# Kernel optimization log

Measured on AMD Instinct MI355X. Metric: run time of the kernel, lower is better.

Reference implementation:

```python
import jax, jax.numpy as jnp
import numpy as np
from jax import lax

E = 256          # embed_dim
D = 2 * E        # d_model
V = 100000       # num_symbols (pad idx = V)
B = 2048         # query batch
NB = 30          # fixed neighbor window (hardcoded in source)
FEW = 3          # hardcoded support set size (view(3,1,2E))
STEPS = 4        # query encoder process steps
EPS = 1e-3       # LayerNormalization eps


def setup_inputs() -> dict:
    key = jax.random.key(0)
    ks = iter(jax.random.split(key, 48))
    def n(shape, s=0.05):
        return jax.random.normal(next(ks), shape, jnp.float32) * s
    inp = {}
    inp["query"] = n((B, D))
    inp["support"] = n((FEW, D))
    inp["query_left_connections"] = jax.random.randint(next(ks), (B, NB, 2), 0, V)
    inp["query_left_degrees"] = jax.random.randint(next(ks), (B,), 1, NB)
    inp["query_right_connections"] = jax.random.randint(next(ks), (B, NB, 2), 0, V)
    inp["query_right_degrees"] = jax.random.randint(next(ks), (B,), 1, NB)
    inp["support_left_connections"] = jax.random.randint(next(ks), (FEW, NB, 2), 0, V)
    inp["support_left_degrees"] = jax.random.randint(next(ks), (FEW,), 1, NB)
    inp["support_right_connections"] = jax.random.randint(next(ks), (FEW, NB, 2), 0, V)
    inp["support_right_degrees"] = jax.random.randint(next(ks), (FEW,), 1, NB)
    # parameters
    inp["emb"] = n((V + 1, E), 0.02).at[V].set(0.0)   # padding_idx row = 0
    inp["naW"] = n((E, D)); inp["naB"] = jnp.zeros((E,), jnp.float32)
    inp["nuW"] = n((1, E)); inp["nuB"] = jnp.zeros((1,), jnp.float32)
    inp["p1W"] = n((2 * D, D)); inp["p1b"] = jnp.zeros((2 * D,), jnp.float32)
    inp["p2W"] = n((D, 2 * D)); inp["p2b"] = jnp.zeros((D,), jnp.float32)
    inp["lnA"] = jnp.ones((D,), jnp.float32); inp["lnB"] = jnp.zeros((D,), jnp.float32)
    inp["encWih"] = n((4 * D, D)); inp["encWhh"] = n((4 * D, D))
    inp["encBih"] = jnp.zeros((4 * D,), jnp.float32); inp["encBhh"] = jnp.zeros((4 * D,), jnp.float32)
    inp["decWih"] = n((4 * D, D)); inp["decWhh"] = n((4 * D, D))
    inp["decBih"] = jnp.zeros((4 * D,), jnp.float32); inp["decBhh"] = jnp.zeros((4 * D,), jnp.float32)
    inp["saW"] = n((E, D)); inp["saB"] = jnp.zeros((E,), jnp.float32)
    inp["suW"] = n((1, E)); inp["suB"] = jnp.zeros((1,), jnp.float32)
    inp["qWih"] = n((8 * D, D)); inp["qWhh"] = n((8 * D, 2 * D))
    inp["qBih"] = jnp.zeros((8 * D,), jnp.float32); inp["qBhh"] = jnp.zeros((8 * D,), jnp.float32)
    return inp


def _lstm_cell(x, h, c, Wih, Whh, bih, bhh):
    g = x @ Wih.T + bih + h @ Whh.T + bhh
    i, f, gg, o = jnp.split(g, 4, axis=-1)
    c = jax.nn.sigmoid(f) * c + jax.nn.sigmoid(i) * jnp.tanh(gg)
    h = jax.nn.sigmoid(o) * jnp.tanh(c)
    return h, c


def _layer_norm(z, a, b):
    # torch.std is unbiased (ddof=1); eps is added to sigma, not variance
    mu = jnp.mean(z, axis=-1, keepdims=True)
    sigma = jnp.std(z, axis=-1, keepdims=True, ddof=1)
    return (z - mu) / (sigma + EPS) * a + b


def _neighbor_encoder(conn, emb, naW, naB, nuW, nuB):
    rel = emb[conn[..., 0]]                 # [N,30,E] gather
    ent = emb[conn[..., 1]]                 # [N,30,E] gather
    cat = jnp.concatenate([rel, ent], -1)   # [N,30,2E]
    out = jnp.tanh(cat @ naW.T + naB)       # [N,30,E]
    att = jax.nn.softmax(out @ nuW.T + nuB, axis=1)  # softmax over 30 neighbors
    agg = jnp.einsum('nk,nke->ne', att[..., 0], ent)  # weighted bmm reduce
    return jnp.tanh(agg)


def _support_encoder(x, p1W, p1b, p2W, p2b, lnA, lnB):
    h = jax.nn.relu(x @ p1W.T + p1b)
    o = h @ p2W.T + p2b
    return _layer_norm(o + x, lnA, lnB)


def reference(query, support,
              query_left_connections, query_left_degrees,
              query_right_connections, query_right_degrees,
              support_left_connections, support_left_degrees,
              support_right_connections, support_right_degrees,
              emb, naW, naB, nuW, nuB, p1W, p1b, p2W, p2b, lnA, lnB,
              encWih, encWhh, encBih, encBhh, decWih, decWhh, decBih, decBhh,
              saW, saB, suW, suB, qWih, qWhh, qBih, qBhh):
    ne = lambda c: _neighbor_encoder(c, emb, naW, naB, nuW, nuB)
    query_neighbor = jnp.concatenate([ne(query_left_connections), ne(query_right_connections)], -1)    # [B,2E]
    support_neighbor = jnp.concatenate([ne(support_left_connections), ne(support_right_connections)], -1)  # [3,2E]

    support_g = _support_encoder(support_neighbor, p1W, p1b, p2W, p2b, lnA, lnB)  # [3,D]
    query_g = _support_encoder(query_neighbor, p1W, p1b, p2W, p2b, lnA, lnB)      # [B,D]

    # set autoencoder: LSTM over the 3 support vectors (seq=3, batch=1)
    support_g_0 = support_g.reshape(FEW, 1, D)
    def enc_step(carry, x):
        h, c = carry
        h, c = _lstm_cell(x, h, c, encWih, encWhh, encBih, encBhh)
        return (h, c), h
    z = jnp.zeros((1, D), support_g.dtype)
    (h_f, c_f), enc_out = lax.scan(enc_step, (z, z), support_g_0)  # enc_out [3,1,D]

    # decoder: feed back its own output 3 times, init from encoder state
    h_d, c_d = h_f, c_f
    x = enc_out[-1]
    outs = []
    for _ in range(FEW):
        h_d, c_d = _lstm_cell(x, h_d, c_d, decWih, decWhh, decBih, decBhh)
        outs.append(h_d)
        x = h_d
    decoder_set = jnp.stack(outs)  # [3,1,D]
    ae_loss = jnp.mean((support_g_0 - lax.stop_gradient(decoder_set)) ** 2)

    sge = support_g_0.reshape(FEW, D) + enc_out.reshape(FEW, D)
    satt = jnp.tanh(sge @ saW.T + saB)                       # [3,E]
    aw = jax.nn.softmax(satt @ suW.T + suB, axis=1)          # softmax over dim of size 1 -> ones (faithful)
    support_g_encoder = (sge.T @ aw).T.reshape(1, D)         # [1,D]

    # query encoder: LSTMCell(D -> 2D) process loop
    h_r = jnp.zeros((query_g.shape[0], 2 * D), query_g.dtype)
    c = jnp.zeros_like(h_r)
    for _ in range(STEPS):
        h_r_, c = _lstm_cell(query_g, h_r, c, qWih, qWhh, qBih, qBhh)
        h = query_g + h_r_[:, :D]
        attn = jax.nn.softmax(h @ support_g_encoder.T, axis=1)  # [B,1] -> ones (faithful)
        r = attn @ support_g_encoder                            # [B,D]
        h_r = jnp.concatenate([h, r], axis=1)
    query_f = h

    matching_scores = (query_f @ support_g_encoder.T)[:, 0]    # [B]
    return (matching_scores, ae_loss, support_g_encoder, query_g)
```

## Files before the change

kernel.cpp:

```cpp
#include <hip/hip_runtime.h>
#include <hip/hip_bf16.h>

typedef unsigned short u16;
typedef __attribute__((ext_vector_type(8))) short bf16x8;
typedef __attribute__((ext_vector_type(4))) float f32x4;
#define MFMA16(a,b,c) __builtin_amdgcn_mfma_f32_16x16x32_bf16(a,b,c,0,0,0)
#define VPAD 100000

__device__ __forceinline__ float sigf(float x){ return 1.0f/(1.0f + __expf(-x)); }
__device__ __forceinline__ float ftanh(float x){
    float ax = fabsf(x);
    float e = __expf(-2.f*ax);
    float r = (1.f - e) / (1.f + e);
    return copysignf(r, x);
}
__device__ __forceinline__ u16 f2b(float f){
    unsigned u = __float_as_uint(f);
    u += 0x7fffu + ((u >> 16) & 1u);
    return (u16)(u >> 16);
}
__device__ __forceinline__ unsigned int pk2(float x, float y){
    return ((unsigned)f2b(y) << 16) | (unsigned)f2b(x);
}
__device__ __forceinline__ float b2f(u16 u){
    return __uint_as_float(((unsigned int)u) << 16);
}
__device__ __forceinline__ uint4 pk8(float4 x, float4 y){
    uint4 o;
    o.x = pk2(x.x,x.y); o.y = pk2(x.z,x.w);
    o.z = pk2(y.x,y.y); o.w = pk2(y.z,y.w);
    return o;
}

__global__ __launch_bounds__(256) void prep_kernel(
    const float* __restrict__ p1W, const float* __restrict__ p2W,
    const float* __restrict__ naW,
    const float* __restrict__ qWih, const float* __restrict__ qWhh,
    const float* __restrict__ qBih, const float* __restrict__ qBhh,
    u16* __restrict__ p1Wb, u16* __restrict__ p2Wb,
    u16* __restrict__ nawf, u16* __restrict__ WihS, u16* __restrict__ WhhS,
    float* __restrict__ bc)
{
    const long gid = (long)blockIdx.x * 256 + threadIdx.x;
    const long E0 = 131072;
    const long E1 = E0 + 131072;
    const long E2 = E1 + 131072;
    const long E3 = E2 + 131072;
    const long E4 = E3 + 16384;
    const long E5 = E4 + 2048;
    if (gid < E0){
        float4 v = reinterpret_cast<const float4*>(p1W)[gid];
        uint2 s; s.x = pk2(v.x,v.y); s.y = pk2(v.z,v.w);
        reinterpret_cast<uint2*>(p1Wb)[gid] = s;
    } else if (gid < E1){
        long i = gid - E0;
        float4 v = reinterpret_cast<const float4*>(p2W)[i];
        uint2 s; s.x = pk2(v.x,v.y); s.y = pk2(v.z,v.w);
        reinterpret_cast<uint2*>(p2Wb)[i] = s;
    } else if (gid < E2){
        long j = gid - E1;
        int n = (int)(j >> 6), c8 = (int)(j & 63);
        int srow = (n & 3) * 1024 + (n >> 2);
        const float* sp = qWih + (size_t)srow * 512 + c8 * 8;
        float4 a = *reinterpret_cast<const float4*>(sp);
        float4 b = *reinterpret_cast<const float4*>(sp + 4);
        *reinterpret_cast<uint4*>(WihS + (size_t)n*512 + c8*8) = pk8(a,b);
    } else if (gid < E3){
        long j = gid - E2;
        int n = (int)(j >> 6), c8 = (int)(j & 63);
        int srow = (n & 3) * 1024 + (n >> 2);
        const float* sp = qWhh + (size_t)srow * 1024 + c8 * 8;
        float4 a = *reinterpret_cast<const float4*>(sp);
        float4 b = *reinterpret_cast<const float4*>(sp + 4);
        *reinterpret_cast<uint4*>(WhhS + (size_t)n*512 + c8*8) = pk8(a,b);
    } else if (gid < E4){
        long j = gid - E3;
        int f = (int)(j >> 6), lane = (int)(j & 63);
        int ks = f >> 4, ig = f & 15;
        int col = lane & 15, quad = lane >> 4;
        int n = ig*16 + col;
        int k0 = ks*32 + quad*8;
        const float* sp = naW + (size_t)n*512 + k0;
        float4 a = *reinterpret_cast<const float4*>(sp);
        float4 b = *reinterpret_cast<const float4*>(sp + 4);
        *reinterpret_cast<uint4*>(nawf + j*8) = pk8(a,b);
    } else if (gid < E5){
        int n = (int)(gid - E4);
        int row = (n & 3) * 1024 + (n >> 2);
        bc[n] = qBih[row] + qBhh[row];
    }
}

__global__ __launch_bounds__(256) void neighbor_v4(
    const int* __restrict__ qL, const int* __restrict__ qR,
    const int* __restrict__ sL, const int* __restrict__ sR,
    const float* __restrict__ emb,
    const u16* __restrict__ nawf,
    const float* __restrict__ naB, const float* __restrict__ nuW,
    const float* __restrict__ nuB,
    float* __restrict__ out, u16* __restrict__ out_bf)
{
    __shared__ __align__(16) u16 frg[32*512];
    __shared__ int relid[2][32];
    __shared__ int entid[2][32];
    __shared__ float logit[2][32];
    __shared__ float att[2][32];

    const int t = threadIdx.x;
    const int row = blockIdx.x;
    if (t < 128){
        int s = t >> 6, j = t & 63;
        int k = j >> 1, which = j & 1;
        const int* conn;
        if (row < 2048) conn = (s ? qR : qL) + (size_t)row * 60;
        else            conn = (s ? sR : sL) + (size_t)(row - 2048) * 60;
        int id = (k < 30) ? conn[k*2 + which] : VPAD;
        if (which) entid[s][k] = id; else relid[s][k] = id;
    }
    if (t >= 128 && t < 192){ int s = (t-128) >> 5; logit[s][(t-128)&31] = 0.f; }
    __syncthreads();

    const int w = t >> 6, lane = t & 63;
    const int col = lane & 15, quad = lane >> 4;

    int gc[8], gk[8], gs[8];
    #pragma unroll
    for (int i = 0; i < 8; i++){
        int idx = i*256 + t;
        gc[i] = idx & 31;
        gk[i] = (idx >> 5) & 31;
        gs[i] = idx >> 10;
    }

    f32x4 acc[4][4] = {};

    #pragma unroll
    for (int p = 0; p < 2; p++){
        #pragma unroll
        for (int i = 0; i < 8; i++){
            int s = gs[i], k = gk[i], c = gc[i];
            int e0 = c*8;
            int id = p ? entid[s][k] : relid[s][k];
            const float* ptr = emb + (size_t)id*256 + e0;
            float4 x = *reinterpret_cast<const float4*>(ptr);
            float4 y = *reinterpret_cast<const float4*>(ptr + 4);
            int ksl = e0 >> 5, q = (e0 >> 3) & 3;
            int mt = k >> 4, cl = k & 15;
            int ln = q*16 + cl;
            u16* dst = frg + ((((s*2 + mt)*8 + ksl)*64) + ln)*8;
            *reinterpret_cast<uint4*>(dst) = pk8(x, y);
        }
        __syncthreads();

        #pragma unroll
        for (int ksl = 0; ksl < 8; ksl++){
            bf16x8 a[4], b[4];
            #pragma unroll
            for (int u = 0; u < 4; u++)
                a[u] = *reinterpret_cast<const bf16x8*>(frg + (((u*8 + ksl)*64) + lane)*8);
            const int ks = p*8 + ksl;
            #pragma unroll
            for (int i = 0; i < 4; i++)
                b[i] = *reinterpret_cast<const bf16x8*>(nawf + ((size_t)(ks*16 + w*4 + i)*64 + lane)*8);
            #pragma unroll
            for (int i = 0; i < 4; i++)
                #pragma unroll
                for (int u = 0; u < 4; u++)
                    acc[u][i] = MFMA16(a[u], b[i], acc[u][i]);
        }
        __syncthreads();
    }

    float nu[4], nbv[4];
    #pragma unroll
    for (int i = 0; i < 4; i++){
        int n = (w*4 + i)*16 + col;
        nu[i] = nuW[n]; nbv[i] = naB[n];
    }
    #pragma unroll
    for (int u = 0; u < 4; u++){
        int s = u >> 1, mt = u & 1;
        #pragma unroll
        for (int r = 0; r < 4; r++){
            int m = mt*16 + quad*4 + r;
            float v = 0.f;
            #pragma unroll
            for (int i = 0; i < 4; i++)
                v += ftanh(acc[u][i][r] + nbv[i]) * nu[i];
            v += __shfl_xor(v, 1); v += __shfl_xor(v, 2);
            v += __shfl_xor(v, 4); v += __shfl_xor(v, 8);
            if (col == 0 && m < 30) atomicAdd(&logit[s][m], v);
        }
    }
    __syncthreads();

    if (t < 2){
        const int s = t;
        const float nub = nuB[0];
        float mx = -1e30f;
        float lg[30];
        #pragma unroll
        for (int k = 0; k < 30; k++){
            float L = logit[s][k] + nub;
            lg[k] = L; mx = fmaxf(mx, L);
        }
        float sm = 0.f;
        #pragma unroll
        for (int k = 0; k < 30; k++){ float e = __expf(lg[k]-mx); att[s][k] = e; sm += e; }
        float inv = 1.f / sm;
        #pragma unroll
        for (int k = 0; k < 30; k++) att[s][k] *= inv;
    }
    __syncthreads();

    const int e = t;
    #pragma unroll
    for (int s = 0; s < 2; s++){
        float agg = 0.f;
        #pragma unroll
        for (int k = 0; k < 30; k++){
            int id = entid[s][k];
            agg += att[s][k] * emb[(size_t)id*256 + e];
        }
        float r = ftanh(agg);
        size_t oi = (size_t)row*512 + s*256 + e;
        out[oi] = r;
        out_bf[oi] = f2b(r);
    }
}

__global__ __launch_bounds__(256) void gemm_tn(
    const u16* __restrict__ A, int lda,
    const u16* __restrict__ B, int ldb,
    const float* __restrict__ bias,
    const float* __restrict__ addD, int ldd,
    float* __restrict__ Cf, u16* __restrict__ Cbf, int ldc,
    int K, int relu,
    float* __restrict__ cst, const float* __restrict__ qgv,
    u16* __restrict__ hout, int gm)
{
    __shared__ __align__(16) u16 As[128][72];
    __shared__ __align__(16) u16 Bs[64][72];
    const int t = threadIdx.x;
    const int m0 = blockIdx.y * 128, n0 = blockIdx.x * 64;
    const int w = t >> 6, lane = t & 63;
    const int col = lane & 15, quad = lane >> 4;
    const int wm = (w & 1) * 64, wn = (w >> 1) * 32;

    int arow[4], aseg[4], brow[2], bseg[2];
    #pragma unroll
    for (int i = 0; i < 4; i++){
        int idx = i*256 + t; arow[i] = idx >> 3; aseg[i] = (idx & 7) * 8;
    }
    #pragma unroll
    for (int i = 0; i < 2; i++){
        int idx = i*256 + t; brow[i] = idx >> 3; bseg[i] = (idx & 7) * 8;
    }

    f32x4 acc[4][2] = {};

    const int KC = K >> 6;
    for (int kc = 0; kc < KC; kc++){
        uint4 av[4], bv[2];
        #pragma unroll
        for (int i = 0; i < 4; i++)
            av[i] = *reinterpret_cast<const uint4*>(A + (size_t)(m0 + arow[i])*lda + kc*64 + aseg[i]);
        #pragma unroll
        for (int i = 0; i < 2; i++)
            bv[i] = *reinterpret_cast<const uint4*>(B + (size_t)(n0 + brow[i])*ldb + kc*64 + bseg[i]);
        __syncthreads();
        #pragma unroll
        for (int i = 0; i < 4; i++)
            *reinterpret_cast<uint4*>(&As[arow[i]][aseg[i]]) = av[i];
        #pragma unroll
        for (int i = 0; i < 2; i++)
            *reinterpret_cast<uint4*>(&Bs[brow[i]][bseg[i]]) = bv[i];
        __syncthreads();
        #pragma unroll
        for (int ks = 0; ks < 2; ks++){
            const int k0 = ks*32 + quad*8;
            bf16x8 af[4], bf[2];
            #pragma unroll
            for (int i = 0; i < 4; i++) af[i] = *reinterpret_cast<const bf16x8*>(&As[wm + i*16 + col][k0]);
            #pragma unroll
            for (int j = 0; j < 2; j++) bf[j] = *reinterpret_cast<const bf16x8*>(&Bs[wn + j*16 + col][k0]);
            #pragma unroll
            for (int i = 0; i < 4; i++)
                #pragma unroll
                for (int j = 0; j < 2; j++)
                    acc[i][j] = MFMA16(af[i], bf[j], acc[i][j]);
        }
    }

    #pragma unroll
    for (int j = 0; j < 2; j++){
        int n = n0 + wn + j*16 + col;
        float bj = bias[n];
        #pragma unroll
        for (int i = 0; i < 4; i++){
            #pragma unroll
            for (int r = 0; r < 4; r++){
                int m = m0 + wm + i*16 + quad*4 + r;
                float v = acc[i][j][r] + bj;
                if (addD) v += addD[(size_t)m*ldd + n];
                if (relu) v = fmaxf(v, 0.f);
                if (Cf)  Cf[(size_t)m*ldc + n] = v;
                if (Cbf) Cbf[(size_t)m*ldc + n] = f2b(v);
                if (gm){
                    float t1 = __shfl_xor(v, 1);
                    float t2 = __shfl_xor(v, 2);
                    float t3 = __shfl_xor(v, 3);
                    if ((lane & 3) == 0){
                        int ci = m*512 + (n >> 2);
                        float c0 = (gm == 2) ? 0.f : cst[ci];
                        float cn = sigf(t1)*c0 + sigf(v)*ftanh(t2);
                        float hn = qgv[ci] + sigf(t3)*ftanh(cn);
                        cst[ci] = cn;
                        hout[ci] = f2b(hn);
                    }
                }
            }
        }
    }
}

__global__ __launch_bounds__(256) void ln_kernel(
    const float* __restrict__ Z, const float* __restrict__ X, int N, int nquery,
    const float* __restrict__ lnA, const float* __restrict__ lnB,
    float* __restrict__ Y, u16* __restrict__ Ybf, float* __restrict__ Ycopy)
{
    const int wv = threadIdx.x >> 6, lane = threadIdx.x & 63;
    const int row = blockIdx.x * 4 + wv;
    if (row >= N) return;
    const float* z = Z + (size_t)row * 512;
    const float* x = X + (size_t)row * 512;
    float v[8];
    float s = 0.f, ss = 0.f;
    {
        float4 z0 = *reinterpret_cast<const float4*>(z + lane*8);
        float4 z1 = *reinterpret_cast<const float4*>(z + lane*8 + 4);
        float4 x0 = *reinterpret_cast<const float4*>(x + lane*8);
        float4 x1 = *reinterpret_cast<const float4*>(x + lane*8 + 4);
        v[0]=z0.x+x0.x; v[1]=z0.y+x0.y; v[2]=z0.z+x0.z; v[3]=z0.w+x0.w;
        v[4]=z1.x+x1.x; v[5]=z1.y+x1.y; v[6]=z1.z+x1.z; v[7]=z1.w+x1.w;
    }
    #pragma unroll
    for (int u = 0; u < 8; u++){ s += v[u]; ss += v[u]*v[u]; }
    #pragma unroll
    for (int d = 1; d < 64; d <<= 1){
        s  += __shfl_xor(s, d);
        ss += __shfl_xor(ss, d);
    }
    float mu  = s * (1.f/512.f);
    float var = (ss - 512.f*mu*mu) * (1.f/511.f);
    float sd  = sqrtf(fmaxf(var, 0.f));
    float inv = 1.f / (sd + 1e-3f);
    float o[8];
    #pragma unroll
    for (int u = 0; u < 8; u++){
        int e = lane*8 + u;
        o[u] = (v[u] - mu) * inv * lnA[e] + lnB[e];
    }
    float* yr = Y + (size_t)row*512 + lane*8;
    *reinterpret_cast<float4*>(yr)     = make_float4(o[0],o[1],o[2],o[3]);
    *reinterpret_cast<float4*>(yr + 4) = make_float4(o[4],o[5],o[6],o[7]);
    if (row < nquery){
        uint4 p;
        p.x = pk2(o[0],o[1]); p.y = pk2(o[2],o[3]);
        p.z = pk2(o[4],o[5]); p.w = pk2(o[6],o[7]);
        *reinterpret_cast<uint4*>(Ybf + (size_t)row*512 + lane*8) = p;
        float* cr = Ycopy + (size_t)row*512 + lane*8;
        *reinterpret_cast<float4*>(cr)     = make_float4(o[0],o[1],o[2],o[3]);
        *reinterpret_cast<float4*>(cr + 4) = make_float4(o[4],o[5],o[6],o[7]);
    }
}

__global__ __launch_bounds__(256) void lstm_small(
    const float* __restrict__ x, const float* __restrict__ hin,
    float* __restrict__ c,
    const float* __restrict__ Wih, const float* __restrict__ Whh,
    const float* __restrict__ bih, const float* __restrict__ bhh,
    float* __restrict__ hout)
{
    __shared__ float xs[512], hs[512];
    __shared__ float gbuf[4][4];
    const int t = threadIdx.x;
    for (int i = t; i < 512; i += 256){ xs[i] = x[i]; hs[i] = hin[i]; }
    __syncthreads();

    const int wd = t >> 6;
    const int lane = t & 63;
    const int g = lane >> 4, p = lane & 15;
    const int d = blockIdx.x*4 + wd;
    const int j = g*512 + d;
    const float4* wi = reinterpret_cast<const float4*>(Wih + (size_t)j*512) + p*8;
    const float4* wh = reinterpret_cast<const float4*>(Whh + (size_t)j*512) + p*8;
    float acc = 0.f;
    #pragma unroll
    for (int q = 0; q < 8; q++){
        float4 wv = wi[q];
        const int kb = p*32 + q*4;
        acc += xs[kb]*wv.x + xs[kb+1]*wv.y + xs[kb+2]*wv.z + xs[kb+3]*wv.w;
        float4 vv = wh[q];
        acc += hs[kb]*vv.x + hs[kb+1]*vv.y + hs[kb+2]*vv.z + hs[kb+3]*vv.w;
    }
    acc += __shfl_xor(acc, 1); acc += __shfl_xor(acc, 2);
    acc += __shfl_xor(acc, 4); acc += __shfl_xor(acc, 8);
    if (p == 0) gbuf[wd][g] = acc + bih[j] + bhh[j];
    __syncthreads();
    if (t < 4){
        int dd = blockIdx.x*4 + t;
        float iv = gbuf[t][0], fv = gbuf[t][1], gv = gbuf[t][2], ov = gbuf[t][3];
        float cn = sigf(fv)*c[dd] + sigf(iv)*ftanh(gv);
        float hn = sigf(ov)*ftanh(cn);
        c[dd] = cn; hout[dd] = hn;
    }
}

__global__ __launch_bounds__(256) void finalize_kernel(
    const float* __restrict__ sg, const float* __restrict__ enc,
    const float* __restrict__ dec, float* __restrict__ sgeenc,
    float* __restrict__ outp)
{
    __shared__ float red[4];
    const int t = threadIdx.x;
    float s = 0.f;
    for (int i = t; i < 1536; i += 256){ float d = sg[i] - dec[i]; s += d*d; }
    s += __shfl_xor(s,1); s += __shfl_xor(s,2); s += __shfl_xor(s,4);
    s += __shfl_xor(s,8); s += __shfl_xor(s,16); s += __shfl_xor(s,32);
    if ((t & 63) == 0) red[t>>6] = s;
    __syncthreads();
    if (t == 0){
        float tot = (red[0]+red[1]+red[2]+red[3]) * (1.f/1536.f);
        outp[2048] = tot;
    }
    for (int d = t; d < 512; d += 256){
        float v = sg[d] + enc[d] + sg[512+d] + enc[512+d] + sg[1024+d] + enc[1024+d];
        sgeenc[d] = v;
        outp[2049 + d] = v;
    }
}

__global__ __launch_bounds__(256) void wvec_kernel(
    const float* __restrict__ qWhh, const float* __restrict__ sge,
    float* __restrict__ wvec)
{
    __shared__ float ss[512];
    const int t = threadIdx.x;
    for (int i = t; i < 512; i += 256) ss[i] = sge[i];
    __syncthreads();
    const int n = blockIdx.x * 256 + t;
    const int row = (n & 3) * 1024 + (n >> 2);
    const float4* w = reinterpret_cast<const float4*>(qWhh + (size_t)row*1024 + 512);
    float acc = 0.f;
    for (int kc = 0; kc < 128; kc++){
        float4 wv = w[kc];
        const int kb = kc*4;
        acc += ss[kb]*wv.x + ss[kb+1]*wv.y + ss[kb+2]*wv.z + ss[kb+3]*wv.w;
    }
    wvec[n] = acc;
}

__global__ __launch_bounds__(256) void scores_kernel(
    const u16* __restrict__ h, const float* __restrict__ sge,
    float* __restrict__ out)
{
    const int wave = threadIdx.x >> 6, lane = threadIdx.x & 63;
    const int row = blockIdx.x * 4 + wave;
    const u16* hr = h + (size_t)row * 512;
    float s = 0.f;
    for (int i = lane; i < 512; i += 64) s += b2f(hr[i]) * sge[i];
    s += __shfl_xor(s,1); s += __shfl_xor(s,2); s += __shfl_xor(s,4);
    s += __shfl_xor(s,8); s += __shfl_xor(s,16); s += __shfl_xor(s,32);
    if (lane == 0) out[row] = s;
}

extern "C" void kernel_launch(void* const* d_in, const int* in_sizes, int n_in,
                              void* d_out, int out_size, void* d_ws, size_t ws_size,
                              hipStream_t stream)
{
    (void)in_sizes; (void)n_in; (void)out_size; (void)ws_size;

    const int* qlc = (const int*)d_in[2];
    const int* qrc = (const int*)d_in[4];
    const int* slc = (const int*)d_in[6];
    const int* src = (const int*)d_in[8];
    const float* emb = (const float*)d_in[10];
    const float* naW = (const float*)d_in[11];
    const float* naB = (const float*)d_in[12];
    const float* nuW = (const float*)d_in[13];
    const float* nuB = (const float*)d_in[14];
    const float* p1W = (const float*)d_in[15], *p1b = (const float*)d_in[16];
    const float* p2W = (const float*)d_in[17], *p2b = (const float*)d_in[18];
    const float* lnA = (const float*)d_in[19], *lnB = (const float*)d_in[20];
    const float* eWih = (const float*)d_in[21], *eWhh = (const float*)d_in[22];
    const float* eBih = (const float*)d_in[23], *eBhh = (const float*)d_in[24];
    const float* dWih = (const float*)d_in[25], *dWhh = (const float*)d_in[26];
    const float* dBih = (const float*)d_in[27], *dBhh = (const float*)d_in[28];
    const float* qWih = (const float*)d_in[33], *qWhh = (const float*)d_in[34];
    const float* qBih = (const float*)d_in[35], *qBhh = (const float*)d_in[36];
    float* out = (float*)d_out;

    float* w = (float*)d_ws;
    size_t off = 0;
    auto alloc = [&](size_t nelem){ float* p = w + off; off += nelem; return p; };
    float* qn    = alloc(2176ull*512);
    float* qg    = alloc(2176ull*512);
    float* enc   = alloc(1536);
    float* dec   = alloc(1536);
    float* zc    = alloc(1024);
    float* sgee  = alloc(512);
    float* wv    = alloc(2048);
    float* bc    = alloc(2048);
    float* nawfF = alloc(65536);
    float* base  = alloc(2048ull*2048);
    float* G     = alloc(2048ull*2048);
    float* cb    = alloc(2048ull*512);
    float* hbfF  = alloc(524288);
    float* p1WbF = alloc(262144);
    float* p2WbF = alloc(262144);
    float* WihSF = alloc(524288);
    float* WhhSF = alloc(524288);

    u16* nawf   = (u16*)nawfF;
    u16* p1Wb   = (u16*)p1WbF;
    u16* p2Wb   = (u16*)p2WbF;
    u16* WihSel = (u16*)WihSF;
    u16* WhhSel = (u16*)WhhSF;
    u16* h_bf   = (u16*)hbfF;
    float* Zq   = base;
    u16* qn_bf  = (u16*)(base + 2097152);
    u16* Hq_bf  = (u16*)G;
    u16* qg_bf  = (u16*)(G + 2097152);
    float* sg   = qg + 2048ull*512;
    float* zbuf = zc;
    float* cst  = zc + 512;

    hipMemsetAsync(zc, 0, 1024*sizeof(float), stream);

    prep_kernel<<<2120, 256, 0, stream>>>(p1W, p2W, naW, qWih, qWhh, qBih, qBhh,
                                          p1Wb, p2Wb, nawf, WihSel, WhhSel, bc);

    neighbor_v4<<<2051, 256, 0, stream>>>(qlc, qrc, slc, src, emb,
                                          nawf, naB, nuW, nuB, qn, qn_bf);

    gemm_tn<<<dim3(16,17), 256, 0, stream>>>(qn_bf, 512, p1Wb, 512, p1b, nullptr, 0,
                                             nullptr, Hq_bf, 1024, 512, 1,
                                             nullptr, nullptr, nullptr, 0);
    gemm_tn<<<dim3(8,17), 256, 0, stream>>>(Hq_bf, 1024, p2Wb, 1024, p2b, nullptr, 0,
                                            Zq, nullptr, 512, 1024, 0,
                                            nullptr, nullptr, nullptr, 0);
    ln_kernel<<<513, 256, 0, stream>>>(Zq, qn, 2051, 2048, lnA, lnB, qg, qg_bf, out + 2561);

    lstm_small<<<128, 256, 0, stream>>>(sg,        zbuf,      cst, eWih, eWhh, eBih, eBhh, enc);
    lstm_small<<<128, 256, 0, stream>>>(sg + 512,  enc,       cst, eWih, eWhh, eBih, eBhh, enc + 512);
    lstm_small<<<128, 256, 0, stream>>>(sg + 1024, enc + 512, cst, eWih, eWhh, eBih, eBhh, enc + 1024);
    lstm_small<<<128, 256, 0, stream>>>(enc + 1024, enc + 1024, cst, dWih, dWhh, dBih, dBhh, dec);
    lstm_small<<<128, 256, 0, stream>>>(dec,        dec,        cst, dWih, dWhh, dBih, dBhh, dec + 512);
    lstm_small<<<128, 256, 0, stream>>>(dec + 512,  dec + 512,  cst, dWih, dWhh, dBih, dBhh, dec + 1024);

    finalize_kernel<<<1, 256, 0, stream>>>(sg, enc, dec, sgee, out);
    wvec_kernel<<<8, 256, 0, stream>>>(qWhh, sgee, wv);

    gemm_tn<<<dim3(32,16), 256, 0, stream>>>(qg_bf, 512, WihSel, 512, bc, nullptr, 0,
                                             base, nullptr, 2048, 512, 0,
                                             cb, qg, h_bf, 2);
    u16* hA = h_bf;
    u16* hB = Hq_bf;
    for (int s = 0; s < 3; s++){
        gemm_tn<<<dim3(32,16), 256, 0, stream>>>(hA, 512, WhhSel, 512, wv, base, 2048,
                                                 nullptr, nullptr, 2048, 512, 0,
                                                 cb, qg, hB, 1);
        u16* tmp = hA; hA = hB; hB = tmp;
    }

    scores_kernel<<<512, 256, 0, stream>>>(hA, sgee, out);
}
```

Before: 669.6 us.

## Swizzle neighbor-fragment LDS layout and stage LSTM gate epilogue through shared memory

The neighbor-encoder's bf16 fragment buffer now uses an XOR swizzle on the lane index by k-slice, which should reduce LDS bank conflicts on writes and reads. The GEMM's fused LSTM-gate epilogue first loads query_g and cell-state tiles into shared memory with coalesced float4 loads. It computes gates against those tiles, then writes c and h back with vectorized stores, replacing scattered per-element global accesses. A standalone gate_kernel is added but appears unused. The shared-buffer reuse relies on As/Bs being large enough and adds extra barriers.

```diff
diff --git a/kernel.cpp b/kernel.cpp
--- a/kernel.cpp
+++ b/kernel.cpp
@@ -146,7 +146,7 @@
             float4 y = *reinterpret_cast<const float4*>(ptr + 4);
             int ksl = e0 >> 5, q = (e0 >> 3) & 3;
             int mt = k >> 4, cl = k & 15;
-            int ln = q*16 + cl;
+            int ln = q*16 + (cl ^ ksl);
             u16* dst = frg + ((((s*2 + mt)*8 + ksl)*64) + ln)*8;
             *reinterpret_cast<uint4*>(dst) = pk8(x, y);
         }
@@ -154,10 +154,11 @@
 
         #pragma unroll
         for (int ksl = 0; ksl < 8; ksl++){
+            const int lnR = (lane & 48) | ((lane & 15) ^ ksl);
             bf16x8 a[4], b[4];
             #pragma unroll
             for (int u = 0; u < 4; u++)
-                a[u] = *reinterpret_cast<const bf16x8*>(frg + (((u*8 + ksl)*64) + lane)*8);
+                a[u] = *reinterpret_cast<const bf16x8*>(frg + (((u*8 + ksl)*64) + lnR)*8);
             const int ks = p*8 + ksl;
             #pragma unroll
             for (int i = 0; i < 4; i++)
@@ -290,6 +291,25 @@
                 for (int j = 0; j < 2; j++)
                     acc[i][j] = MFMA16(af[i], bf[j], acc[i][j]);
         }
+    }
+
+    float* qb   = reinterpret_cast<float*>(&As[0][0]);
+    float* cbuf = qb + 2048;
+    u16*   hbuf = &Bs[0][0];
+    const int d0 = n0 >> 2;
+    if (gm){
+        __syncthreads();
+        #pragma unroll
+        for (int u = 0; u < 2; u++){
+            int idx = u*256 + t;
+            int m = idx >> 2, dq = (idx & 3)*4;
+            *reinterpret_cast<float4*>(&qb[m*16 + dq]) =
+                *reinterpret_cast<const float4*>(&qgv[(size_t)(m0+m)*512 + d0 + dq]);
+            if (gm == 1)
+                *reinterpret_cast<float4*>(&cbuf[m*16 + dq]) =
+                    *reinterpret_cast<const float4*>(&cst[(size_t)(m0+m)*512 + d0 + dq]);
+        }
+        __syncthreads();
     }
 
     #pragma unroll
@@ -311,15 +331,30 @@
                     float t2 = __shfl_xor(v, 2);
                     float t3 = __shfl_xor(v, 3);
                     if ((lane & 3) == 0){
-                        int ci = m*512 + (n >> 2);
-                        float c0 = (gm == 2) ? 0.f : cst[ci];
+                        int mloc = wm + i*16 + quad*4 + r;
+                        int dloc = (wn + j*16 + col) >> 2;
+                        int si = mloc*16 + dloc;
+                        float c0 = (gm == 2) ? 0.f : cbuf[si];
                         float cn = sigf(t1)*c0 + sigf(v)*ftanh(t2);
-                        float hn = qgv[ci] + sigf(t3)*ftanh(cn);
-                        cst[ci] = cn;
-                        hout[ci] = f2b(hn);
+                        float hn = qb[si] + sigf(t3)*ftanh(cn);
+                        cbuf[si] = cn;
+                        hbuf[si] = f2b(hn);
                     }
                 }
             }
+        }
+    }
+
+    if (gm){
+        __syncthreads();
+        #pragma unroll
+        for (int u = 0; u < 2; u++){
+            int idx = u*256 + t;
+            int m = idx >> 2, dq = (idx & 3)*4;
+            *reinterpret_cast<float4*>(&cst[(size_t)(m0+m)*512 + d0 + dq]) =
+                *reinterpret_cast<const float4*>(&cbuf[m*16 + dq]);
+            *reinterpret_cast<uint2*>(&hout[(size_t)(m0+m)*512 + d0 + dq]) =
+                *reinterpret_cast<const uint2*>(&hbuf[m*16 + dq]);
         }
     }
 }
@@ -459,6 +494,18 @@
         acc += ss[kb]*wv.x + ss[kb+1]*wv.y + ss[kb+2]*wv.z + ss[kb+3]*wv.w;
     }
     wvec[n] = acc;
+}
+
+__global__ __launch_bounds__(256) void gate_kernel(
+    const float* __restrict__ G, const float* __restrict__ qg,
+    float* __restrict__ c, u16* __restrict__ h_bf)
+{
+    const int idx = blockIdx.x * 256 + threadIdx.x;
+    const int b = idx >> 9, d = idx & 511;
+    float4 g4 = *reinterpret_cast<const float4*>(G + (size_t)b*2048 + d*4);
+    float cn = sigf(g4.y)*c[idx] + sigf(g4.x)*ftanh(g4.z);
+    float hn = qg[idx] + sigf(g4.w)*ftanh(cn);
+    c[idx] = cn; h_bf[idx] = f2b(hn);
 }
 
 __global__ __launch_bounds__(256) void scores_kernel(
```

New measurement: 722.7 us. 1.08x slower.
